# Kernel optimization log

Hardware: AMD Instinct MI355X
Metric: run time of the kernel (lower is better)

Reference implementation:

```python
import jax, jax.numpy as jnp
import numpy as np

N_NODES = 100000


def _gcn_conv(x, W, b, src, dst, ew, num_nodes):
    # PyG GCNConv: symmetric normalization with self-loops already included
    # in (src, dst, ew). deg computed on destination (col) index.
    deg = jax.ops.segment_sum(ew, dst, num_segments=num_nodes)  # [N]
    dinv = jnp.where(deg > 0, jax.lax.rsqrt(deg), 0.0)          # [N]
    norm = dinv[src] * ew * dinv[dst]                           # [E]
    h = x @ W                                                   # [N, out]
    msg = h[src] * norm[:, None]                                # [E, out] gather+scale
    out = jax.ops.segment_sum(msg, dst, num_segments=num_nodes) # scatter-add
    return out + b


def setup_inputs() -> dict:
    key = jax.random.key(0)
    k = jax.random.split(key, 8)
    in_c, hid_c, out_c = 128, 128, 64
    E, EL = 1600000, 200000
    x = jax.random.normal(k[0], (N_NODES, in_c), dtype=jnp.float32)
    edge_index = jax.random.randint(k[1], (2, E), 0, N_NODES, dtype=jnp.int64)
    edge_weight = jax.random.uniform(k[2], (E,), dtype=jnp.float32)
    edge_label_index = jax.random.randint(k[3], (2, EL), 0, N_NODES, dtype=jnp.int64)
    # Glorot-ish params
    W1 = jax.random.normal(k[4], (in_c, hid_c), dtype=jnp.float32) / np.sqrt(in_c)
    b1 = jnp.zeros((hid_c,), dtype=jnp.float32)
    W2 = jax.random.normal(k[5], (hid_c, out_c), dtype=jnp.float32) / np.sqrt(hid_c)
    b2 = jnp.zeros((out_c,), dtype=jnp.float32)
    return {"x": x, "edge_index": edge_index, "edge_weight": edge_weight,
            "edge_label_index": edge_label_index,
            "W1": W1, "b1": b1, "W2": W2, "b2": b2}


def reference(x, edge_index, edge_weight, edge_label_index, W1, b1, W2, b2):
    n = x.shape[0]
    # add self-loops (weight 1.0), static shape
    loop = jnp.arange(n, dtype=edge_index.dtype)
    src = jnp.concatenate([edge_index[0], loop])
    dst = jnp.concatenate([edge_index[1], loop])
    ew = jnp.concatenate([edge_weight, jnp.ones((n,), dtype=edge_weight.dtype)])
    h = jax.nn.relu(_gcn_conv(x, W1, b1, src, dst, ew, n))
    z = _gcn_conv(h, W2, b2, src, dst, ew, n)          # [N, out_c]
    # decode: edge dot-product
    return (z[edge_label_index[0]] * z[edge_label_index[1]]).sum(axis=-1)
```

## Files before the change

kernel.cpp:

```cpp
#include <hip/hip_runtime.h>
#include <hip/hip_fp16.h>
#include <math.h>

__device__ __forceinline__ float2 h2f2(unsigned int u) {
    __half2 h = *reinterpret_cast<__half2*>(&u);
    return __half22float2(h);
}
__device__ __forceinline__ unsigned int f2h2(float a, float b) {
    __half2 h = __floats2half2_rn(a, b);
    return *reinterpret_cast<unsigned int*>(&h);
}

__global__ __launch_bounds__(256) void gemm128_hist_kernel(
        const float* __restrict__ X, const float* __restrict__ W, __half* __restrict__ Y, int n,
        const int* __restrict__ dst, const float* __restrict__ ew,
        int* __restrict__ cnt, float* __restrict__ wsum, int* __restrict__ rank, int E) {
    constexpr int CG  = 32;
    constexpr int M   = 64;
    constexpr int RT  = 8;
    constexpr int KC  = 32;
    constexpr int LDX = 132;
    __shared__ float  Xl[M * LDX];
    __shared__ float4 Wl[KC * CG];

    const int bid = blockIdx.x;
    const int t = threadIdx.x;
    const int EPB = (E + (int)gridDim.x - 1) / (int)gridDim.x;
    const int eBeg = bid * EPB;
    const int eEnd = min(eBeg + EPB, E);

    if ((bid & 1) == 0) {
        for (int e = eBeg + t; e < eEnd; e += 256) {
            int d = dst[e];
            rank[e] = atomicAdd(&cnt[d], 1);
            atomicAdd(&wsum[d], ew[e]);
        }
    }

    int row0 = bid * M;
    {
        const float4* Xg = (const float4*)X;
        for (int f = t; f < M * 32; f += 256) {
            int r = f >> 5, c4 = f & 31;
            int gr = row0 + r;
            float4 v = make_float4(0.f, 0.f, 0.f, 0.f);
            if (gr < n) v = Xg[(size_t)gr * 32 + c4];
            *(float4*)&Xl[r * LDX + c4 * 4] = v;
        }
    }

    int cg = t % CG;
    int r0 = (t / CG) * RT;

    float4 acc[RT];
#pragma unroll
    for (int r = 0; r < RT; r++) acc[r] = make_float4(0.f, 0.f, 0.f, 0.f);

    const float4* Wg = (const float4*)W;
    for (int kc = 0; kc < 128; kc += KC) {
        __syncthreads();
        for (int f = t; f < KC * CG; f += 256)
            Wl[f] = Wg[(size_t)kc * CG + f];
        __syncthreads();
#pragma unroll 4
        for (int k = 0; k < KC; k += 4) {
            float4 b0 = Wl[(k + 0) * CG + cg];
            float4 b1 = Wl[(k + 1) * CG + cg];
            float4 b2 = Wl[(k + 2) * CG + cg];
            float4 b3 = Wl[(k + 3) * CG + cg];
#pragma unroll
            for (int r = 0; r < RT; r++) {
                float4 a = *(float4*)&Xl[(r0 + r) * LDX + kc + k];
                acc[r].x += a.x * b0.x + a.y * b1.x + a.z * b2.x + a.w * b3.x;
                acc[r].y += a.x * b0.y + a.y * b1.y + a.z * b2.y + a.w * b3.y;
                acc[r].z += a.x * b0.z + a.y * b1.z + a.z * b2.z + a.w * b3.z;
                acc[r].w += a.x * b0.w + a.y * b1.w + a.z * b2.w + a.w * b3.w;
            }
        }
    }

#pragma unroll
    for (int r = 0; r < RT; r++) {
        int gr = row0 + r0 + r;
        if (gr < n) {
            uint2 u = make_uint2(f2h2(acc[r].x, acc[r].y), f2h2(acc[r].z, acc[r].w));
            *(uint2*)&Y[(size_t)gr * 128 + cg * 4] = u;
        }
    }

    if (bid & 1) {
        for (int e = eBeg + t; e < eEnd; e += 256) {
            int d = dst[e];
            rank[e] = atomicAdd(&cnt[d], 1);
            atomicAdd(&wsum[d], ew[e]);
        }
    }
}

__global__ __launch_bounds__(256) void scan_block(const int* __restrict__ in, int* __restrict__ out,
                                                  int* __restrict__ bsum, int n) {
    __shared__ int s[256];
    int tid = threadIdx.x;
    int base = blockIdx.x * 1024 + tid * 4;
    int a0 = (base + 0 < n) ? in[base + 0] : 0;
    int a1 = (base + 1 < n) ? in[base + 1] : 0;
    int a2 = (base + 2 < n) ? in[base + 2] : 0;
    int a3 = (base + 3 < n) ? in[base + 3] : 0;
    int tsum = a0 + a1 + a2 + a3;
    s[tid] = tsum;
    __syncthreads();
    for (int off = 1; off < 256; off <<= 1) {
        int v = (tid >= off) ? s[tid - off] : 0;
        __syncthreads();
        s[tid] += v;
        __syncthreads();
    }
    int texcl = s[tid] - tsum;
    if (base + 0 < n) out[base + 0] = texcl;
    if (base + 1 < n) out[base + 1] = texcl + a0;
    if (base + 2 < n) out[base + 2] = texcl + a0 + a1;
    if (base + 3 < n) out[base + 3] = texcl + a0 + a1 + a2;
    if (tid == 255) bsum[blockIdx.x] = s[255];
}

__global__ __launch_bounds__(256) void scan_bsums(int* __restrict__ bsum, int nb) {
    __shared__ int s[256];
    __shared__ int carry_s;
    int tid = threadIdx.x;
    if (tid == 0) carry_s = 0;
    __syncthreads();
    for (int base = 0; base < nb; base += 256) {
        int v = (base + tid < nb) ? bsum[base + tid] : 0;
        int orig = v;
        s[tid] = v;
        __syncthreads();
        for (int off = 1; off < 256; off <<= 1) {
            int u = (tid >= off) ? s[tid - off] : 0;
            __syncthreads();
            s[tid] += u;
            __syncthreads();
        }
        int carry = carry_s;
        int excl = s[tid] - orig + carry;
        if (base + tid < nb) bsum[base + tid] = excl;
        int tot = s[255];
        __syncthreads();
        if (tid == 0) carry_s = carry + tot;
        __syncthreads();
    }
}

__global__ void scan_add(int* __restrict__ rowptr, const int* __restrict__ bscan, int n) {
    int t = blockIdx.x * blockDim.x + threadIdx.x;
    if (t < n) rowptr[t] += bscan[t >> 10];
}

__global__ void dinv_kernel(const float* __restrict__ wsum, float* __restrict__ dinv, int n) {
    int i = blockIdx.x * blockDim.x + threadIdx.x;
    if (i >= n) return;
    dinv[i] = 1.0f / sqrtf(wsum[i] + 1.0f);
}

__global__ void scatter_pairs(const int* __restrict__ src, const int* __restrict__ dst,
                              const float* __restrict__ ew, const int* __restrict__ rowptr,
                              const int* __restrict__ rank, const float* __restrict__ dinv,
                              int2* __restrict__ pairs, int E) {
    int e = blockIdx.x * blockDim.x + threadIdx.x;
    if (e >= E) return;
    int d = dst[e];
    int s = src[e];
    int p = rowptr[d] + rank[e];
    pairs[p] = make_int2(s, __float_as_int(ew[e] * dinv[s]));
}

__global__ __launch_bounds__(512, 4) void gather_mv_kernel(const __half* __restrict__ H,
                                                           const int* __restrict__ rowptr,
                                                           const int2* __restrict__ pairs,
                                                           const float* __restrict__ dinv,
                                                           const float* __restrict__ bias,
                                                           const float* __restrict__ W2,
                                                           __half* __restrict__ Z, int n) {
    __shared__ float h1s[16 * 128];
    __shared__ float w2s[128 * 64];
    const int t = threadIdx.x;
    const int nl = t >> 5;
    const int c4 = t & 31;
    const int node = blockIdx.x * 16 + nl;

    {
        const float4* W2g = (const float4*)W2;
        float4* w2s4 = (float4*)w2s;
#pragma unroll
        for (int f = 0; f < 4; f++) w2s4[f * 512 + t] = W2g[f * 512 + t];
    }

    float4 acc[4];
#pragma unroll
    for (int i = 0; i < 4; i++) acc[i] = make_float4(0.f, 0.f, 0.f, 0.f);

    float di = 0.f;
    int beg = 0, end = 0;
    if (node < n) {
        beg = rowptr[node]; end = rowptr[node + 1];
        di = dinv[node];
        uint2 hv = *(const uint2*)&H[(size_t)node * 128 + c4 * 4];
        float2 f01 = h2f2(hv.x), f23 = h2f2(hv.y);
        acc[0].x = f01.x * di; acc[0].y = f01.y * di;
        acc[0].z = f23.x * di; acc[0].w = f23.y * di;
    }

    if (beg < end) {
        int2 pc[8];
#pragma unroll
        for (int i = 0; i < 8; i++) {
            int jj = beg + i;
            pc[i] = pairs[jj < end ? jj : beg];
        }
        for (int j = beg; j < end; j += 8) {
            uint2 v[8];
#pragma unroll
            for (int i = 0; i < 8; i++)
                v[i] = *(const uint2*)&H[(size_t)(unsigned)pc[i].x * 128 + c4 * 4];
            int2 pn[8];
            int jn = j + 8;
#pragma unroll
            for (int i = 0; i < 8; i++) {
                int jj = jn + i;
                pn[i] = pairs[jj < end ? jj : beg];
            }
#pragma unroll
            for (int i = 0; i < 8; i++) {
                float w = (j + i < end) ? __int_as_float(pc[i].y) : 0.f;
                float2 g01 = h2f2(v[i].x), g23 = h2f2(v[i].y);
                acc[i & 3].x += g01.x * w; acc[i & 3].y += g01.y * w;
                acc[i & 3].z += g23.x * w; acc[i & 3].w += g23.y * w;
            }
#pragma unroll
            for (int i = 0; i < 8; i++) pc[i] = pn[i];
        }
    }

    float4 a0 = make_float4(0.f, 0.f, 0.f, 0.f);
    if (node < n) {
        float4 bb = ((const float4*)bias)[c4];
        a0.x = fmaxf(((acc[0].x + acc[1].x) + (acc[2].x + acc[3].x)) * di + bb.x, 0.f);
        a0.y = fmaxf(((acc[0].y + acc[1].y) + (acc[2].y + acc[3].y)) * di + bb.y, 0.f);
        a0.z = fmaxf(((acc[0].z + acc[1].z) + (acc[2].z + acc[3].z)) * di + bb.z, 0.f);
        a0.w = fmaxf(((acc[0].w + acc[1].w) + (acc[2].w + acc[3].w)) * di + bb.w, 0.f);
    }
    *(float4*)&h1s[nl * 128 + c4 * 4] = a0;
    __syncthreads();

    float z0 = 0.f, z1 = 0.f;
    const float* hrow = &h1s[nl * 128];
    const float2* w2c = (const float2*)w2s;
#pragma unroll 8
    for (int k = 0; k < 128; k++) {
        float hk = hrow[k];
        float2 w = w2c[k * 32 + c4];
        z0 += hk * w.x;
        z1 += hk * w.y;
    }
    if (node < n) *(unsigned int*)&Z[(size_t)node * 64 + c4 * 2] = f2h2(z0, z1);
}

__global__ __launch_bounds__(256, 4) void gather_reduce64(const __half* __restrict__ H,
                                                          const int* __restrict__ rowptr,
                                                          const int2* __restrict__ pairs,
                                                          const float* __restrict__ dinv,
                                                          const float* __restrict__ bias,
                                                          __half* __restrict__ out, int n) {
    constexpr int TPN = 16;
    int t = blockIdx.x * blockDim.x + threadIdx.x;
    int node = t / TPN;
    int c4 = t % TPN;
    if (node >= n) return;
    int beg = rowptr[node], end = rowptr[node + 1];
    float di = dinv[node];
    float4 bb = ((const float4*)bias)[c4];
    float4 acc[4];
    {
        uint2 hv = *(const uint2*)&H[(size_t)node * 64 + c4 * 4];
        float2 f01 = h2f2(hv.x), f23 = h2f2(hv.y);
        acc[0].x = f01.x * di; acc[0].y = f01.y * di;
        acc[0].z = f23.x * di; acc[0].w = f23.y * di;
    }
#pragma unroll
    for (int i = 1; i < 4; i++) acc[i] = make_float4(0.f, 0.f, 0.f, 0.f);

    if (beg < end) {
        int2 pc[8];
#pragma unroll
        for (int i = 0; i < 8; i++) {
            int jj = beg + i;
            pc[i] = pairs[jj < end ? jj : beg];
        }
        for (int j = beg; j < end; j += 8) {
            uint2 v[8];
#pragma unroll
            for (int i = 0; i < 8; i++)
                v[i] = *(const uint2*)&H[(size_t)(unsigned)pc[i].x * 64 + c4 * 4];
            int2 pn[8];
            int jn = j + 8;
#pragma unroll
            for (int i = 0; i < 8; i++) {
                int jj = jn + i;
                pn[i] = pairs[jj < end ? jj : beg];
            }
#pragma unroll
            for (int i = 0; i < 8; i++) {
                float w = (j + i < end) ? __int_as_float(pc[i].y) : 0.f;
                float2 g01 = h2f2(v[i].x), g23 = h2f2(v[i].y);
                acc[i & 3].x += g01.x * w; acc[i & 3].y += g01.y * w;
                acc[i & 3].z += g23.x * w; acc[i & 3].w += g23.y * w;
            }
#pragma unroll
            for (int i = 0; i < 8; i++) pc[i] = pn[i];
        }
    }

    float4 r;
    r.x = ((acc[0].x + acc[1].x) + (acc[2].x + acc[3].x)) * di + bb.x;
    r.y = ((acc[0].y + acc[1].y) + (acc[2].y + acc[3].y)) * di + bb.y;
    r.z = ((acc[0].z + acc[1].z) + (acc[2].z + acc[3].z)) * di + bb.z;
    r.w = ((acc[0].w + acc[1].w) + (acc[2].w + acc[3].w)) * di + bb.w;
    uint2 u = make_uint2(f2h2(r.x, r.y), f2h2(r.z, r.w));
    *(uint2*)&out[(size_t)node * 64 + c4 * 4] = u;
}

__global__ void decode_kernel(const __half* __restrict__ Z, const int* __restrict__ ea,
                              const int* __restrict__ eb, float* __restrict__ out, int L) {
    int t = blockIdx.x * blockDim.x + threadIdx.x;
    int e = t >> 4;
    int c = (t & 15) << 2;
    if (e >= L) return;
    uint2 ua = *(const uint2*)&Z[(size_t)ea[e] * 64 + c];
    uint2 ub = *(const uint2*)&Z[(size_t)eb[e] * 64 + c];
    float2 a01 = h2f2(ua.x), a23 = h2f2(ua.y);
    float2 b01 = h2f2(ub.x), b23 = h2f2(ub.y);
    float p = a01.x * b01.x + a01.y * b01.y + a23.x * b23.x + a23.y * b23.y;
    p += __shfl_xor(p, 1);
    p += __shfl_xor(p, 2);
    p += __shfl_xor(p, 4);
    p += __shfl_xor(p, 8);
    if ((t & 15) == 0) out[e] = p;
}

extern "C" void kernel_launch(void* const* d_in, const int* in_sizes, int n_in,
                              void* d_out, int out_size, void* d_ws, size_t ws_size,
                              hipStream_t stream) {
    const float* x   = (const float*)d_in[0];
    const int*   ei  = (const int*)d_in[1];
    const float* ew  = (const float*)d_in[2];
    const int*   eli = (const int*)d_in[3];
    const float* W1  = (const float*)d_in[4];
    const float* b1  = (const float*)d_in[5];
    const float* W2  = (const float*)d_in[6];
    const float* b2  = (const float*)d_in[7];
    float* out = (float*)d_out;

    const int N = in_sizes[0] / 128;
    const int E = in_sizes[2];
    const int L = in_sizes[3] / 2;
    const int NP = ((N + 255) / 256) * 256;

    float* ws     = (float*)d_ws;
    float* dinv   = ws;
    float* wsum   = ws + NP;
    int*   cnt    = (int*)(wsum + NP);
    int*   rowptr = cnt + NP;
    int*   bsum   = rowptr + NP;
    int*   rank   = bsum + 1024;
    int2*  pairs  = (int2*)(rank + E);
    __half* A     = (__half*)(pairs + E);
    __half* B     = (__half*)((float*)(pairs + E) + (size_t)NP * 128);
    __half* Zf    = A;

    const int n1 = N + 1;
    const int nb = (n1 + 1023) / 1024;

    hipMemsetAsync(wsum, 0, ((size_t)NP + (size_t)n1) * 4, stream);

    const int Gg = (N + 63) / 64;
    gemm128_hist_kernel<<<Gg, 256, 0, stream>>>(x, W1, A, N, ei + E, ew, cnt, wsum, rank, E);

    dinv_kernel<<<(N + 255) / 256, 256, 0, stream>>>(wsum, dinv, N);

    scan_block<<<nb, 256, 0, stream>>>(cnt, rowptr, bsum, n1);
    scan_bsums<<<1, 256, 0, stream>>>(bsum, nb);
    scan_add<<<(n1 + 255) / 256, 256, 0, stream>>>(rowptr, bsum, n1);
    scatter_pairs<<<(E + 255) / 256, 256, 0, stream>>>(ei, ei + E, ew, rowptr, rank, dinv, pairs, E);

    gather_mv_kernel<<<(N + 15) / 16, 512, 0, stream>>>(A, rowptr, pairs, dinv, b1, W2, B, N);

    gather_reduce64<<<(N * 16 + 255) / 256, 256, 0, stream>>>(B, rowptr, pairs, dinv, b2, Zf, N);

    decode_kernel<<<(L * 16 + 255) / 256, 256, 0, stream>>>(Zf, eli, eli + L, out, L);
}
```

Before: 471.1 us.

## Compute degree from CSR segments instead of float atomics on wsum

Drops the float atomicAdd on per-destination weight sums during the histogram pass. Degrees are instead reduced per node over the CSR-sorted pairs after scatter, and a new pass premultiplies the edge weights by dinv[src]. This removes E float atomics but adds two extra kernels that reread the pairs array, one of which reads and rewrites all E entries.

```diff
diff --git a/kernel.cpp b/kernel.cpp
--- a/kernel.cpp
+++ b/kernel.cpp
@@ -13,8 +13,7 @@
 
 __global__ __launch_bounds__(256) void gemm128_hist_kernel(
         const float* __restrict__ X, const float* __restrict__ W, __half* __restrict__ Y, int n,
-        const int* __restrict__ dst, const float* __restrict__ ew,
-        int* __restrict__ cnt, float* __restrict__ wsum, int* __restrict__ rank, int E) {
+        const int* __restrict__ dst, int* __restrict__ cnt, int* __restrict__ rank, int E) {
     constexpr int CG  = 32;
     constexpr int M   = 64;
     constexpr int RT  = 8;
@@ -30,11 +29,8 @@
     const int eEnd = min(eBeg + EPB, E);
 
     if ((bid & 1) == 0) {
-        for (int e = eBeg + t; e < eEnd; e += 256) {
-            int d = dst[e];
-            rank[e] = atomicAdd(&cnt[d], 1);
-            atomicAdd(&wsum[d], ew[e]);
-        }
+        for (int e = eBeg + t; e < eEnd; e += 256)
+            rank[e] = atomicAdd(&cnt[dst[e]], 1);
     }
 
     int row0 = bid * M;
@@ -89,11 +85,8 @@
     }
 
     if (bid & 1) {
-        for (int e = eBeg + t; e < eEnd; e += 256) {
-            int d = dst[e];
-            rank[e] = atomicAdd(&cnt[d], 1);
-            atomicAdd(&wsum[d], ew[e]);
-        }
+        for (int e = eBeg + t; e < eEnd; e += 256)
+            rank[e] = atomicAdd(&cnt[dst[e]], 1);
     }
 }
 
@@ -155,22 +148,32 @@
     if (t < n) rowptr[t] += bscan[t >> 10];
 }
 
-__global__ void dinv_kernel(const float* __restrict__ wsum, float* __restrict__ dinv, int n) {
-    int i = blockIdx.x * blockDim.x + threadIdx.x;
-    if (i >= n) return;
-    dinv[i] = 1.0f / sqrtf(wsum[i] + 1.0f);
-}
-
 __global__ void scatter_pairs(const int* __restrict__ src, const int* __restrict__ dst,
                               const float* __restrict__ ew, const int* __restrict__ rowptr,
-                              const int* __restrict__ rank, const float* __restrict__ dinv,
-                              int2* __restrict__ pairs, int E) {
+                              const int* __restrict__ rank, int2* __restrict__ pairs, int E) {
     int e = blockIdx.x * blockDim.x + threadIdx.x;
     if (e >= E) return;
     int d = dst[e];
-    int s = src[e];
     int p = rowptr[d] + rank[e];
-    pairs[p] = make_int2(s, __float_as_int(ew[e] * dinv[s]));
+    pairs[p] = make_int2(src[e], __float_as_int(ew[e]));
+}
+
+__global__ void deg_dinv_kernel(const int2* __restrict__ pairs, const int* __restrict__ rowptr,
+                                float* __restrict__ dinv, int n) {
+    int i = blockIdx.x * blockDim.x + threadIdx.x;
+    if (i >= n) return;
+    int beg = rowptr[i], end = rowptr[i + 1];
+    float s = 0.f;
+    for (int j = beg; j < end; j++) s += __int_as_float(pairs[j].y);
+    dinv[i] = 1.0f / sqrtf(s + 1.0f);
+}
+
+__global__ void premul_kernel(int2* __restrict__ pairs, const float* __restrict__ dinv, int E) {
+    int e = blockIdx.x * blockDim.x + threadIdx.x;
+    if (e >= E) return;
+    int2 p = pairs[e];
+    p.y = __float_as_int(__int_as_float(p.y) * dinv[p.x]);
+    pairs[e] = p;
 }
 
 __global__ __launch_bounds__(512, 4) void gather_mv_kernel(const __half* __restrict__ H,
@@ -366,8 +369,7 @@
 
     float* ws     = (float*)d_ws;
     float* dinv   = ws;
-    float* wsum   = ws + NP;
-    int*   cnt    = (int*)(wsum + NP);
+    int*   cnt    = (int*)(ws + NP);
     int*   rowptr = cnt + NP;
     int*   bsum   = rowptr + NP;
     int*   rank   = bsum + 1024;
@@ -379,17 +381,17 @@
     const int n1 = N + 1;
     const int nb = (n1 + 1023) / 1024;
 
-    hipMemsetAsync(wsum, 0, ((size_t)NP + (size_t)n1) * 4, stream);
+    hipMemsetAsync(cnt, 0, (size_t)n1 * 4, stream);
 
     const int Gg = (N + 63) / 64;
-    gemm128_hist_kernel<<<Gg, 256, 0, stream>>>(x, W1, A, N, ei + E, ew, cnt, wsum, rank, E);
-
-    dinv_kernel<<<(N + 255) / 256, 256, 0, stream>>>(wsum, dinv, N);
+    gemm128_hist_kernel<<<Gg, 256, 0, stream>>>(x, W1, A, N, ei + E, cnt, rank, E);
 
     scan_block<<<nb, 256, 0, stream>>>(cnt, rowptr, bsum, n1);
     scan_bsums<<<1, 256, 0, stream>>>(bsum, nb);
     scan_add<<<(n1 + 255) / 256, 256, 0, stream>>>(rowptr, bsum, n1);
-    scatter_pairs<<<(E + 255) / 256, 256, 0, stream>>>(ei, ei + E, ew, rowptr, rank, dinv, pairs, E);
+    scatter_pairs<<<(E + 255) / 256, 256, 0, stream>>>(ei, ei + E, ew, rowptr, rank, pairs, E);
+    deg_dinv_kernel<<<(N + 255) / 256, 256, 0, stream>>>(pairs, rowptr, dinv, N);
+    premul_kernel<<<(E + 255) / 256, 256, 0, stream>>>(pairs, dinv, E);
 
     gather_mv_kernel<<<(N + 15) / 16, 512, 0, stream>>>(A, rowptr, pairs, dinv, b1, W2, B, N);
 
```

Measured after the change: 421.8 us. 10.5% less time.
